# Optimization experiments

Measured on AMD Instinct MI355X. Metric: run time of the kernel, lower is better.

## Reference

```python
import jax, jax.numpy as jnp
import numpy as np

DIM = 384
HEADS = 12
WS = (2, 7, 7)
SS = (1, 3, 3)


def _rel_position_index(ws):
    coords = np.stack(np.meshgrid(np.arange(ws[0]), np.arange(ws[1]), np.arange(ws[2]), indexing='ij'))
    cf = coords.reshape(3, -1)                      # (3, N)
    rc = cf[:, :, None] - cf[:, None, :]            # (3, N, N)
    rc = rc.transpose(1, 2, 0).astype(np.int64)     # (N, N, 3)
    rc[..., 0] += ws[0] - 1
    rc[..., 1] += ws[1] - 1
    rc[..., 2] += ws[2] - 1
    rc[..., 0] *= (2 * ws[1] - 1) * (2 * ws[2] - 1)
    rc[..., 1] *= 2 * ws[2] - 1
    return rc.sum(-1)                               # (N, N)


def _compute_mask(D, H, W, ws, ss):
    img = np.zeros((1, D, H, W, 1), np.float32)
    cnt = 0
    for d in (slice(0, -ws[0]), slice(-ws[0], -ss[0]), slice(-ss[0], None)):
        for h in (slice(0, -ws[1]), slice(-ws[1], -ss[1]), slice(-ss[1], None)):
            for w in (slice(0, -ws[2]), slice(-ws[2], -ss[2]), slice(-ss[2], None)):
                img[:, d, h, w, :] = cnt
                cnt += 1
    x = img.reshape(1, D // ws[0], ws[0], H // ws[1], ws[1], W // ws[2], ws[2], 1)
    mw = x.transpose(0, 1, 3, 5, 2, 4, 6, 7).reshape(-1, ws[0] * ws[1] * ws[2])  # (nW, N)
    am = mw[:, None, :] - mw[:, :, None]
    return jnp.asarray(np.where(am != 0, -100.0, 0.0).astype(np.float32))  # (nW, N, N)


def _window_partition(x, ws):
    B, D, H, W, C = x.shape
    x = x.reshape(B, D // ws[0], ws[0], H // ws[1], ws[1], W // ws[2], ws[2], C)
    return x.transpose(0, 1, 3, 5, 2, 4, 6, 7).reshape(-1, ws[0] * ws[1] * ws[2], C)


def _window_reverse(win, ws, B, D, H, W):
    x = win.reshape(B, D // ws[0], H // ws[1], W // ws[2], ws[0], ws[1], ws[2], -1)
    return x.transpose(0, 1, 4, 2, 5, 3, 6, 7).reshape(B, D, H, W, -1)


def _ln(x, g, b, eps=1e-5):
    mu = x.mean(-1, keepdims=True)
    var = ((x - mu) ** 2).mean(-1, keepdims=True)
    return (x - mu) * jax.lax.rsqrt(var + eps) * g + b


def setup_inputs() -> dict:
    key = jax.random.key(0)
    ks = jax.random.split(key, 8)
    C = DIM
    Ch = int(4.0 * C)
    s = lambda k, shape: jax.random.normal(k, shape, dtype=jnp.float32) * 0.02
    nbias = (2 * WS[0] - 1) * (2 * WS[1] - 1) * (2 * WS[2] - 1)
    return dict(
        x=jax.random.normal(ks[0], (4, 8, 56, 56, C), dtype=jnp.float32),
        norm1_g=jnp.ones((C,), jnp.float32), norm1_b=jnp.zeros((C,), jnp.float32),
        qkv_w=s(ks[1], (3 * C, C)), qkv_b=jnp.zeros((3 * C,), jnp.float32),
        rpb_table=s(ks[2], (nbias, HEADS)),
        proj_w=s(ks[3], (C, C)), proj_b=jnp.zeros((C,), jnp.float32),
        norm2_g=jnp.ones((C,), jnp.float32), norm2_b=jnp.zeros((C,), jnp.float32),
        fc1_w=s(ks[4], (Ch, C)), fc1_b=jnp.zeros((Ch,), jnp.float32),
        fc2_w=s(ks[5], (C, Ch)), fc2_b=jnp.zeros((C,), jnp.float32),
    )


def reference(x, norm1_g, norm1_b, qkv_w, qkv_b, rpb_table, proj_w, proj_b,
              norm2_g, norm2_b, fc1_w, fc1_b, fc2_w, fc2_b):
    B, D, H, W, C = x.shape
    ws, ss = WS, SS
    hd = C // HEADS
    N = ws[0] * ws[1] * ws[2]

    shortcut = x
    h = _ln(x, norm1_g, norm1_b)
    # cyclic shift (no padding needed: D,H,W are window multiples)
    h = jnp.roll(h, shift=(-ss[0], -ss[1], -ss[2]), axis=(1, 2, 3))
    xw = _window_partition(h, ws)                       # (B_, N, C)
    B_ = xw.shape[0]

    qkv = (xw @ qkv_w.T + qkv_b).reshape(B_, N, 3, HEADS, hd).transpose(2, 0, 3, 1, 4)
    q, k, v = qkv[0], qkv[1], qkv[2]                    # (B_, heads, N, hd)
    attn = jnp.einsum('bhnd,bhmd->bhnm', q * (hd ** -0.5), k)

    rpi = _rel_position_index(ws)                       # (N, N) static
    bias = rpb_table[rpi.reshape(-1)].reshape(N, N, HEADS).transpose(2, 0, 1)
    attn = attn + bias[None]

    mask = _compute_mask(D, H, W, ws, ss)               # (nW, N, N)
    nW = mask.shape[0]
    attn = attn.reshape(B_ // nW, nW, HEADS, N, N) + mask[None, :, None]
    attn = jax.nn.softmax(attn.reshape(-1, HEADS, N, N), axis=-1)

    out = jnp.einsum('bhnm,bhmd->bhnd', attn, v).transpose(0, 2, 1, 3).reshape(B_, N, C)
    out = out @ proj_w.T + proj_b

    h = _window_reverse(out, ws, B, D, H, W)
    h = jnp.roll(h, shift=(ss[0], ss[1], ss[2]), axis=(1, 2, 3))
    x = shortcut + h

    y = _ln(x, norm2_g, norm2_b)
    y = jax.nn.gelu(y @ fc1_w.T + fc1_b, approximate=False) @ fc2_w.T + fc2_b
    return x + y
```

## Files before the change

kernel.cpp:

```cpp
#include <hip/hip_runtime.h>
#include <hip/hip_bf16.h>
#include <cmath>

typedef __hip_bfloat16 bf16;
typedef __attribute__((ext_vector_type(8))) short s16x8;
typedef __attribute__((ext_vector_type(4))) float f32x4v;

__device__ __forceinline__ float bf2f(bf16 v){ return __bfloat162float(v); }
__device__ __forceinline__ bf16  f2bf(float v){ return __float2bfloat16(v); }

__device__ __forceinline__ void gload16(const void* g, void* l){
  __builtin_amdgcn_global_load_lds((const __attribute__((address_space(1))) void*)g,
                                   (__attribute__((address_space(3))) void*)l,
                                   16, 0, 0);
}

__device__ __forceinline__ int xcd_swizzle(int bid, int nb){
  int q = nb >> 3, r = nb & 7;
  int xcd = bid & 7, idx = bid >> 3;
  return (xcd < r) ? (xcd*(q+1) + idx) : (r + xcd*q + idx);
}

__device__ __forceinline__ float gelu_f(float v){
  float y = 0.797884561f*(v + 0.044715f*v*v*v);
  float e = __expf(-2.f*y);
  return v * __builtin_amdgcn_rcpf(1.f + e);
}

__global__ void k_f2bf(const float* __restrict__ in, bf16* __restrict__ out, int n){
  int i = blockIdx.x*256 + threadIdx.x;
  if (i < n) out[i] = f2bf(in[i]);
}

__global__ void k_comb(const float* __restrict__ rpb, float* __restrict__ comb){
  int idx = blockIdx.x*256 + threadIdx.x;
  int col = idx & 127, row = (idx>>7)&127, clshead = idx>>14;
  int cls = clshead/12, head = clshead - cls*12;
  float v;
  if (row >= 98) v = 0.f;
  else if (col >= 98) v = -10000.f;
  else {
    int qd = row/49, qr = row%49, qh = qr/7, qw = qr%7;
    int kd = col/49, kr = col%49, kh = kr/7, kw = kr%7;
    int pbq = qd*169 + qh*13 + qw;
    int pbk = kd*169 + kh*13 + kw;
    int lq, lk;
    {
      int ld = (cls&4) ? (qd==0?1:2) : 0;
      int lh = (cls&2) ? (qh<4?1:2) : 0;
      int lw = (cls&1) ? (qw<4?1:2) : 0;
      lq = ld*9+lh*3+lw;
    }
    {
      int ld = (cls&4) ? (kd==0?1:2) : 0;
      int lh = (cls&2) ? (kh<4?1:2) : 0;
      int lw = (cls&1) ? (kw<4?1:2) : 0;
      lk = ld*9+lh*3+lw;
    }
    float bias = rpb[(pbq-pbk+253)*12 + head];
    v = bias + ((lq!=lk) ? -100.f : 0.f);
  }
  comb[idx] = v;
}

__global__ __launch_bounds__(256)
void k_ln1(const float* __restrict__ x, const float* __restrict__ g,
           const float* __restrict__ b, bf16* __restrict__ xw, long tbase)
{
  int tl = blockIdx.x*4 + (threadIdx.x>>6);
  long t = tbase + tl;
  int lane = threadIdx.x & 63;
  int win = (int)(t / 98), n = (int)(t % 98);
  int batch = win>>8;
  int wq = win & 7, hq = (win>>3)&7, dq = (win>>6)&3;
  int dr = n/49, rem = n%49, hr = rem/7, wr = rem%7;
  int d = dq*2+dr, h = hq*7+hr, w = wq*7+wr;
  int sd = (d+1)&7;
  int sh = h+3; if (sh>=56) sh-=56;
  int sw = w+3; if (sw>=56) sw-=56;
  const float* row = x + ((size_t)(((batch*8+sd)*56+sh)*56+sw))*384;
  float v[6]; float s=0.f, ss=0.f;
  int c0 = lane*6;
  #pragma unroll
  for (int i=0;i<6;++i){ float f = row[c0+i]; v[i]=f; s+=f; ss+=f*f; }
  #pragma unroll
  for (int o=32;o>0;o>>=1){ s += __shfl_xor(s,o); ss += __shfl_xor(ss,o); }
  float mu = s*(1.f/384.f);
  float var = ss*(1.f/384.f) - mu*mu;
  float rstd = rsqrtf(var + 1e-5f);
  bf16* orow = xw + (size_t)tl*384;
  #pragma unroll
  for (int i=0;i<6;++i){ int c=c0+i; orow[c] = f2bf((v[i]-mu)*rstd*g[c] + b[c]); }
}

__global__ __launch_bounds__(256)
void k_scatter_ln2(const bf16* __restrict__ projout, const float* __restrict__ x,
                   const float* __restrict__ g, const float* __restrict__ b,
                   float* __restrict__ x2, bf16* __restrict__ ln2,
                   long tbase, long lnbase)
{
  int tl = blockIdx.x*4 + (threadIdx.x>>6);
  long t = tbase + tl;
  int lane = threadIdx.x & 63;
  int win = (int)(t/98), n = (int)(t%98);
  int batch = win>>8;
  int wq = win&7, hq=(win>>3)&7, dq=(win>>6)&3;
  int dr=n/49, rem=n%49, hr=rem/7, wr=rem%7;
  int d=dq*2+dr, h=hq*7+hr, w=wq*7+wr;
  int sd=(d+1)&7;
  int sh=h+3; if(sh>=56)sh-=56;
  int sw=w+3; if(sw>=56)sw-=56;
  size_t nat = (size_t)(sd*56+sh)*56 + sw;
  size_t nrow = (size_t)batch*25088 + nat;
  const float* xrow = x + nrow*384;
  const bf16* prow = projout + (size_t)tl*384;
  float* x2row = x2 + nrow*384;
  bf16* lrow = ln2 + (nrow - (size_t)lnbase)*384;
  int c0 = lane*6;
  float v[6]; float s=0.f, ss=0.f;
  #pragma unroll
  for (int i=0;i<6;++i){
    float f = xrow[c0+i] + bf2f(prow[c0+i]);
    v[i]=f; s+=f; ss+=f*f;
    x2row[c0+i] = f;
  }
  #pragma unroll
  for (int o=32;o>0;o>>=1){ s+=__shfl_xor(s,o); ss+=__shfl_xor(ss,o); }
  float mu=s*(1.f/384.f), var=ss*(1.f/384.f)-mu*mu, rstd=rsqrtf(var+1e-5f);
  #pragma unroll
  for (int i=0;i<6;++i){ int c=c0+i; lrow[c]=f2bf((v[i]-mu)*rstd*g[c]+b[c]); }
}

template<int EPI, int KT>
__global__ __launch_bounds__(256, 2)
void k_gemm(const bf16* __restrict__ A, const bf16* __restrict__ B,
            const float* __restrict__ bias, const float* __restrict__ resid,
            void* __restrict__ outp, int N, int nx)
{
  constexpr int K = KT*32;
  __shared__ __align__(16) bf16 As[2][256*32];
  __shared__ __align__(16) bf16 Bs[2][128*32];
  const int tid = threadIdx.x;
  const int wave = tid>>6, lane = tid&63;
  const int wg = xcd_swizzle(blockIdx.x, gridDim.x);
  const int tn = wg % nx, tm = wg / nx;
  const int wm = wave>>1, wn = wave&1;
  const int fr = lane & 15, l4 = lane>>4;

  f32x4v acc[8][4];
  #pragma unroll
  for (int i=0;i<8;++i)
    #pragma unroll
    for (int j=0;j<4;++j)
      #pragma unroll
      for (int e=0;e<4;++e) acc[i][j][e] = 0.f;

  const int srow0 = lane>>2;
  const int scol_sw = (((lane&3) ^ ((lane>>3)&3)))*8;
  const bf16* gA = A + ((size_t)tm*256 + wave*16 + srow0)*K + scol_sw;
  const bf16* gB = B + ((size_t)tn*128 + wave*16 + srow0)*K + scol_sw;

  auto stage = [&](int buf, int koff){
    #pragma unroll
    for (int j=0;j<4;++j)
      gload16(gA + (size_t)(64*j)*K + koff, &As[buf][j*2048 + wave*512]);
    #pragma unroll
    for (int j=0;j<2;++j)
      gload16(gB + (size_t)(64*j)*K + koff, &Bs[buf][j*2048 + wave*512]);
  };

  stage(0, 0);

  const int fko_sw = ((l4 ^ ((fr>>1)&3)))*8;

  #pragma unroll 2
  for (int kt=0; kt<KT; ++kt){
    asm volatile("s_waitcnt vmcnt(0) lgkmcnt(0)" ::: "memory");
    __builtin_amdgcn_s_barrier();
    if (kt+1 < KT) stage((kt+1)&1, (kt+1)*32);
    const bf16* Ab = As[kt&1];
    const bf16* Bb = Bs[kt&1];
    s16x8 af[8], bfr[4];
    #pragma unroll
    for (int i=0;i<4;++i)
      bfr[i] = *(const s16x8*)&Bb[(wn*64 + i*16 + fr)*32 + fko_sw];
    #pragma unroll
    for (int i=0;i<8;++i)
      af[i] = *(const s16x8*)&Ab[(wm*128 + i*16 + fr)*32 + fko_sw];
    #pragma unroll
    for (int mi=0;mi<8;++mi)
      #pragma unroll
      for (int ni=0;ni<4;++ni)
        acc[mi][ni] = __builtin_amdgcn_mfma_f32_16x16x32_bf16(af[mi], bfr[ni], acc[mi][ni], 0,0,0);
    __builtin_amdgcn_s_barrier();
  }

  #pragma unroll
  for (int mi=0;mi<8;++mi){
    #pragma unroll
    for (int ni=0;ni<4;++ni){
      int col = tn*128 + wn*64 + ni*16 + fr;
      float bv = bias[col];
      int rowb = tm*256 + wm*128 + mi*16 + l4*4;
      #pragma unroll
      for (int r=0;r<4;++r){
        size_t idx = (size_t)(rowb+r)*N + col;
        float v = acc[mi][ni][r] + bv;
        if (EPI==0){
          ((bf16*)outp)[idx] = f2bf(v);
        } else if (EPI==1){
          ((bf16*)outp)[idx] = f2bf(gelu_f(v));
        } else if (EPI==3){
          if (col < 384) v *= 0.17677669529663687f;
          ((bf16*)outp)[idx] = f2bf(v);
        } else {
          ((float*)outp)[idx] = v + resid[idx];
        }
      }
    }
  }
}

__global__ __launch_bounds__(256)
void k_attn(const bf16* __restrict__ qkv, const float* __restrict__ comb,
            bf16* __restrict__ outp)
{
  const int wg   = xcd_swizzle(blockIdx.x, gridDim.x);
  const int head = wg % 12;
  const int win  = wg / 12;
  const int tid  = threadIdx.x;
  const int wave = tid>>6;
  const int lane = tid&63;
  const int l15 = lane & 15, l4 = lane>>4;
  __shared__ __align__(16) bf16 Vt[32*136];
  __shared__ __align__(16) bf16 P_buf[4][16*40];

  const int wq = win&7, hq=(win>>3)&7, dq=(win>>6)&3;
  const int cls = ((dq==3)?4:0) | ((hq==7)?2:0) | ((wq==7)?1:0);
  const float* combbase = comb + (size_t)(cls*12+head)*128*128;
  const bf16* qkvw_ = qkv + (size_t)win*98*1152;

  for (int i = tid; i < 512; i += 256){
    int m = i>>2, d0 = (i&3)*8;
    int mc = m>97 ? 97 : m;
    s16x8 v = *(const s16x8*)(qkvw_ + (size_t)mc*1152 + 768 + head*32 + d0);
    #pragma unroll
    for (int e=0;e<8;++e){ short sv = v[e]; Vt[(d0+e)*136 + m] = *(bf16*)&sv; }
  }
  s16x8 kb[8];
  #pragma unroll
  for (int j=0;j<8;++j){
    int tok = j*16 + l15; if (tok>97) tok = 97;
    kb[j] = *(const s16x8*)(qkvw_ + (size_t)tok*1152 + 384 + head*32 + l4*8);
  }
  __syncthreads();

  const int c0 = wave*32;
  bf16* Pw = P_buf[wave];
  #pragma unroll
  for (int mi=0;mi<2;++mi){
    int q = c0 + mi*16 + l15; if (q>97) q=97;
    s16x8 aq = *(const s16x8*)(qkvw_ + (size_t)q*1152 + head*32 + l4*8);
    f32x4v s[8];
    const float* cb = combbase + (size_t)(c0+mi*16+l4*4)*128 + l15;
    #pragma unroll
    for (int j=0;j<8;++j){
      f32x4v ci = { cb[j*16], cb[j*16+128], cb[j*16+256], cb[j*16+384] };
      s[j] = __builtin_amdgcn_mfma_f32_16x16x32_bf16(aq, kb[j], ci, 0,0,0);
    }
    float rinv[4];
    #pragma unroll
    for (int r=0;r<4;++r){
      float mx = s[0][r];
      #pragma unroll
      for (int j=1;j<8;++j) mx = fmaxf(mx, s[j][r]);
      mx = fmaxf(mx, __shfl_xor(mx,1));
      mx = fmaxf(mx, __shfl_xor(mx,2));
      mx = fmaxf(mx, __shfl_xor(mx,4));
      mx = fmaxf(mx, __shfl_xor(mx,8));
      float sum = 0.f;
      #pragma unroll
      for (int j=0;j<8;++j){ float e = __expf(s[j][r]-mx); s[j][r]=e; sum+=e; }
      sum += __shfl_xor(sum,1);
      sum += __shfl_xor(sum,2);
      sum += __shfl_xor(sum,4);
      sum += __shfl_xor(sum,8);
      rinv[r] = 1.f/sum;
    }
    f32x4v oacc[2] = {{0.f,0.f,0.f,0.f},{0.f,0.f,0.f,0.f}};
    #pragma unroll
    for (int ks=0; ks<4; ++ks){
      #pragma unroll
      for (int jj=0;jj<2;++jj)
        #pragma unroll
        for (int r=0;r<4;++r)
          Pw[(l4*4+r)*40 + jj*16 + l15] = f2bf(s[ks*2+jj][r]);
      s16x8 pa = *(const s16x8*)&Pw[l15*40 + l4*8];
      #pragma unroll
      for (int ni=0;ni<2;++ni){
        s16x8 vb = *(const s16x8*)&Vt[(ni*16+l15)*136 + ks*32 + l4*8];
        oacc[ni] = __builtin_amdgcn_mfma_f32_16x16x32_bf16(pa, vb, oacc[ni], 0,0,0);
      }
    }
    #pragma unroll
    for (int r=0;r<4;++r){
      int qo = c0 + mi*16 + l4*4 + r;
      if (qo < 98){
        bf16* orow = outp + ((size_t)win*98 + qo)*384 + head*32;
        #pragma unroll
        for (int ni=0;ni<2;++ni)
          orow[ni*16+l15] = f2bf(oacc[ni][r]*rinv[r]);
      }
    }
  }
}

extern "C" void kernel_launch(void* const* d_in, const int* in_sizes, int n_in,
                              void* d_out, int out_size, void* d_ws, size_t ws_size,
                              hipStream_t stream)
{
  const float* x     = (const float*)d_in[0];
  const float* n1g   = (const float*)d_in[1];
  const float* n1b   = (const float*)d_in[2];
  const float* qkvw  = (const float*)d_in[3];
  const float* qkvbv = (const float*)d_in[4];
  const float* rpb   = (const float*)d_in[5];
  const float* projw = (const float*)d_in[6];
  const float* projb = (const float*)d_in[7];
  const float* n2g   = (const float*)d_in[8];
  const float* n2b   = (const float*)d_in[9];
  const float* fc1w  = (const float*)d_in[10];
  const float* fc1b  = (const float*)d_in[11];
  const float* fc2w  = (const float*)d_in[12];
  const float* fc2b  = (const float*)d_in[13];
  float* out = (float*)d_out;

  char* ws = (char*)d_ws;
  size_t off = 0;
  auto alloc = [&](size_t bytes)->char*{
    char* p = ws + off; off += (bytes + 255) & ~(size_t)255; return p;
  };
  bf16*  wqkv  = (bf16*)alloc((size_t)1152*384*2);
  bf16*  wproj = (bf16*)alloc((size_t)384*384*2);
  bf16*  wfc1  = (bf16*)alloc((size_t)1536*384*2);
  bf16*  wfc2  = (bf16*)alloc((size_t)384*1536*2);
  float* comb  = (float*)alloc((size_t)96*128*128*4);

  k_f2bf<<<(1152*384+255)/256,256,0,stream>>>(qkvw, wqkv, 1152*384);
  k_f2bf<<<(384*384+255)/256,256,0,stream>>>(projw, wproj, 384*384);
  k_f2bf<<<(1536*384+255)/256,256,0,stream>>>(fc1w, wfc1, 1536*384);
  k_f2bf<<<(384*1536+255)/256,256,0,stream>>>(fc2w, wfc2, 384*1536);
  k_comb<<<6144,256,0,stream>>>(rpb, comb);

  const size_t fused_need = off + ((size_t)100352*384*2 + 255 & ~(size_t)255)
                                + ((size_t)100352*1536*2 + 255 & ~(size_t)255)
                                + ((size_t)100352*384*2 + 255 & ~(size_t)255);
  if (ws_size >= fused_need){
    bf16* xw   = (bf16*)alloc((size_t)100352*384*2);
    bf16* bufA = (bf16*)alloc((size_t)100352*1536*2);
    bf16* ln2  = (bf16*)alloc((size_t)100352*384*2);
    bf16* attno = bufA + (size_t)100352*1152;
    bf16* projo = xw;

    k_ln1<<<25088,256,0,stream>>>(x, n1g, n1b, xw, 0L);
    k_gemm<3,12><<<392*9,256,0,stream>>>(xw, wqkv, qkvbv, nullptr, bufA, 1152, 9);
    k_attn<<<12*1024,256,0,stream>>>(bufA, comb, attno);
    k_gemm<0,12><<<392*3,256,0,stream>>>(attno, wproj, projb, nullptr, projo, 384, 3);
    k_scatter_ln2<<<25088,256,0,stream>>>(projo, x, n2g, n2b, out, ln2, 0L, 0L);
    k_gemm<1,12><<<392*12,256,0,stream>>>(ln2, wfc1, fc1b, nullptr, bufA, 1536, 12);
    k_gemm<2,48><<<392*3,256,0,stream>>>(bufA, wfc2, fc2b, out, (void*)out, 384, 3);
  } else {
    bf16* xw   = (bf16*)alloc((size_t)25088*384*2);
    bf16* bufA = (bf16*)alloc((size_t)25088*1536*2);
    bf16* ln2  = (bf16*)alloc((size_t)25088*384*2);
    bf16* attno = bufA + (size_t)25088*1152;
    bf16* projo = xw;
    for (int b=0; b<4; ++b){
      long tbase = (long)b*25088;
      k_ln1<<<6272,256,0,stream>>>(x, n1g, n1b, xw, tbase);
      k_gemm<3,12><<<98*9,256,0,stream>>>(xw, wqkv, qkvbv, nullptr, bufA, 1152, 9);
      k_attn<<<12*256,256,0,stream>>>(bufA, comb, attno);
      k_gemm<0,12><<<98*3,256,0,stream>>>(attno, wproj, projb, nullptr, projo, 384, 3);
      k_scatter_ln2<<<6272,256,0,stream>>>(projo, x, n2g, n2b, out, ln2, tbase, tbase);
      k_gemm<1,12><<<98*12,256,0,stream>>>(ln2, wfc1, fc1b, nullptr, bufA, 1536, 12);
      float* resid = out + (size_t)b*25088*384;
      k_gemm<2,48><<<98*3,256,0,stream>>>(bufA, wfc2, fc2b, resid, (void*)resid, 384, 3);
    }
  }
}
```

Measured before the change: 954.3 us.

## Fuse projection GEMM with residual add, window reverse and LayerNorm2

Replaces the projection GEMM plus separate scatter/LN2 kernel with one 512-thread kernel where each block computes 128 full rows of 384 output columns. It adds bias and the shortcut, writes the residual to its unshifted position, reduces row statistics through shared memory and writes the normalized bf16 LN2 input. This removes the bf16 projection intermediate round trip and one launch. The four weight-conversion launches are also merged into one. The cost is a large per-block tile with one block per CU, which may reduce occupancy and overlap.

```diff
diff --git a/kernel.cpp b/kernel.cpp
--- a/kernel.cpp
+++ b/kernel.cpp
@@ -27,9 +27,17 @@
   return v * __builtin_amdgcn_rcpf(1.f + e);
 }
 
-__global__ void k_f2bf(const float* __restrict__ in, bf16* __restrict__ out, int n){
+__global__ void k_f2bf4(const float* __restrict__ s0, const float* __restrict__ s1,
+                        const float* __restrict__ s2, const float* __restrict__ s3,
+                        bf16* __restrict__ out){
   int i = blockIdx.x*256 + threadIdx.x;
-  if (i < n) out[i] = f2bf(in[i]);
+  if (i >= 1769472) return;
+  float v;
+  if      (i <  442368) v = s0[i];
+  else if (i <  589824) v = s1[i -  442368];
+  else if (i < 1179648) v = s2[i -  589824];
+  else                  v = s3[i - 1179648];
+  out[i] = f2bf(v);
 }
 
 __global__ void k_comb(const float* __restrict__ rpb, float* __restrict__ comb){
@@ -93,44 +101,6 @@
   for (int i=0;i<6;++i){ int c=c0+i; orow[c] = f2bf((v[i]-mu)*rstd*g[c] + b[c]); }
 }
 
-__global__ __launch_bounds__(256)
-void k_scatter_ln2(const bf16* __restrict__ projout, const float* __restrict__ x,
-                   const float* __restrict__ g, const float* __restrict__ b,
-                   float* __restrict__ x2, bf16* __restrict__ ln2,
-                   long tbase, long lnbase)
-{
-  int tl = blockIdx.x*4 + (threadIdx.x>>6);
-  long t = tbase + tl;
-  int lane = threadIdx.x & 63;
-  int win = (int)(t/98), n = (int)(t%98);
-  int batch = win>>8;
-  int wq = win&7, hq=(win>>3)&7, dq=(win>>6)&3;
-  int dr=n/49, rem=n%49, hr=rem/7, wr=rem%7;
-  int d=dq*2+dr, h=hq*7+hr, w=wq*7+wr;
-  int sd=(d+1)&7;
-  int sh=h+3; if(sh>=56)sh-=56;
-  int sw=w+3; if(sw>=56)sw-=56;
-  size_t nat = (size_t)(sd*56+sh)*56 + sw;
-  size_t nrow = (size_t)batch*25088 + nat;
-  const float* xrow = x + nrow*384;
-  const bf16* prow = projout + (size_t)tl*384;
-  float* x2row = x2 + nrow*384;
-  bf16* lrow = ln2 + (nrow - (size_t)lnbase)*384;
-  int c0 = lane*6;
-  float v[6]; float s=0.f, ss=0.f;
-  #pragma unroll
-  for (int i=0;i<6;++i){
-    float f = xrow[c0+i] + bf2f(prow[c0+i]);
-    v[i]=f; s+=f; ss+=f*f;
-    x2row[c0+i] = f;
-  }
-  #pragma unroll
-  for (int o=32;o>0;o>>=1){ s+=__shfl_xor(s,o); ss+=__shfl_xor(ss,o); }
-  float mu=s*(1.f/384.f), var=ss*(1.f/384.f)-mu*mu, rstd=rsqrtf(var+1e-5f);
-  #pragma unroll
-  for (int i=0;i<6;++i){ int c=c0+i; lrow[c]=f2bf((v[i]-mu)*rstd*g[c]+b[c]); }
-}
-
 template<int EPI, int KT>
 __global__ __launch_bounds__(256, 2)
 void k_gemm(const bf16* __restrict__ A, const bf16* __restrict__ B,
@@ -221,6 +191,136 @@
   }
 }
 
+template<int KT>
+__global__ __launch_bounds__(512, 1)
+void k_projln2(const bf16* __restrict__ A, const bf16* __restrict__ B,
+               const float* __restrict__ bias, const float* __restrict__ x,
+               const float* __restrict__ g, const float* __restrict__ b2,
+               float* __restrict__ outx, bf16* __restrict__ ln2,
+               long tbase, long lnbase)
+{
+  constexpr int K = KT*32;
+  __shared__ __align__(16) bf16 As[2][128*32];
+  __shared__ __align__(16) bf16 Bs[2][384*32];
+  __shared__ float redS[128][4];
+  __shared__ float redQ[128][4];
+  const int tid = threadIdx.x;
+  const int wave = tid>>6, lane = tid&63;
+  const int tm = xcd_swizzle(blockIdx.x, gridDim.x);
+  const int wm = wave>>2, wn = wave&3;
+  const int fr = lane & 15, l4 = lane>>4;
+
+  f32x4v acc[4][6];
+  #pragma unroll
+  for (int i=0;i<4;++i)
+    #pragma unroll
+    for (int j=0;j<6;++j)
+      #pragma unroll
+      for (int e=0;e<4;++e) acc[i][j][e] = 0.f;
+
+  const int srow0 = lane>>2;
+  const int scol_sw = (((lane&3) ^ ((lane>>3)&3)))*8;
+  const bf16* gA = A + ((size_t)tm*128 + wave*16 + srow0)*K + scol_sw;
+  const bf16* gB = B + ((size_t)(wave*16) + srow0)*K + scol_sw;
+
+  auto stage = [&](int buf, int koff){
+    gload16(gA + koff, &As[buf][wave*512]);
+    #pragma unroll
+    for (int j=0;j<3;++j)
+      gload16(gB + (size_t)(128*j)*K + koff, &Bs[buf][(j*128 + wave*16)*32]);
+  };
+
+  stage(0, 0);
+  const int fko_sw = ((l4 ^ ((fr>>1)&3)))*8;
+
+  #pragma unroll 2
+  for (int kt=0; kt<KT; ++kt){
+    asm volatile("s_waitcnt vmcnt(0) lgkmcnt(0)" ::: "memory");
+    __builtin_amdgcn_s_barrier();
+    if (kt+1 < KT) stage((kt+1)&1, (kt+1)*32);
+    const bf16* Ab = As[kt&1];
+    const bf16* Bb = Bs[kt&1];
+    s16x8 af[4], bfr[6];
+    #pragma unroll
+    for (int i=0;i<6;++i)
+      bfr[i] = *(const s16x8*)&Bb[(wn*96 + i*16 + fr)*32 + fko_sw];
+    #pragma unroll
+    for (int i=0;i<4;++i)
+      af[i] = *(const s16x8*)&Ab[(wm*64 + i*16 + fr)*32 + fko_sw];
+    #pragma unroll
+    for (int mi=0;mi<4;++mi)
+      #pragma unroll
+      for (int ni=0;ni<6;++ni)
+        acc[mi][ni] = __builtin_amdgcn_mfma_f32_16x16x32_bf16(af[mi], bfr[ni], acc[mi][ni], 0,0,0);
+    __builtin_amdgcn_s_barrier();
+  }
+
+  float bv[6];
+  #pragma unroll
+  for (int ni=0;ni<6;++ni) bv[ni] = bias[wn*96 + ni*16 + fr];
+
+  long nr[4][4];
+  #pragma unroll
+  for (int mi=0;mi<4;++mi){
+    #pragma unroll
+    for (int r=0;r<4;++r){
+      int lrow = wm*64 + mi*16 + l4*4 + r;
+      int ti = (int)(tbase + (long)tm*128 + lrow);
+      int win = ti/98, n = ti - win*98;
+      int batch = win>>8;
+      int wq = win&7, hq = (win>>3)&7, dq = (win>>6)&3;
+      int dr = n/49, rem = n - dr*49, hr = rem/7, wr = rem - hr*7;
+      int d = dq*2+dr, h = hq*7+hr, w = wq*7+wr;
+      int sd = (d+1)&7;
+      int sh = h+3; if (sh>=56) sh-=56;
+      int sw = w+3; if (sw>=56) sw-=56;
+      long nrow = (long)batch*25088 + (long)(sd*56+sh)*56 + sw;
+      nr[mi][r] = nrow;
+      const float* xrow = x + (size_t)nrow*384;
+      float* orow = outx + (size_t)nrow*384;
+      float s = 0.f, q = 0.f;
+      #pragma unroll
+      for (int ni=0;ni<6;++ni){
+        int col = wn*96 + ni*16 + fr;
+        float hvl = acc[mi][ni][r] + bv[ni] + xrow[col];
+        orow[col] = hvl;
+        acc[mi][ni][r] = hvl;
+        s += hvl; q += hvl*hvl;
+      }
+      s += __shfl_xor(s,1); q += __shfl_xor(q,1);
+      s += __shfl_xor(s,2); q += __shfl_xor(q,2);
+      s += __shfl_xor(s,4); q += __shfl_xor(q,4);
+      s += __shfl_xor(s,8); q += __shfl_xor(q,8);
+      if (fr == 0){ redS[lrow][wn] = s; redQ[lrow][wn] = q; }
+    }
+  }
+  __syncthreads();
+  float gv[6], b2v[6];
+  #pragma unroll
+  for (int ni=0;ni<6;++ni){
+    int col = wn*96 + ni*16 + fr;
+    gv[ni] = g[col]; b2v[ni] = b2[col];
+  }
+  #pragma unroll
+  for (int mi=0;mi<4;++mi){
+    #pragma unroll
+    for (int r=0;r<4;++r){
+      int lrow = wm*64 + mi*16 + l4*4 + r;
+      float S = redS[lrow][0] + redS[lrow][1] + redS[lrow][2] + redS[lrow][3];
+      float Q = redQ[lrow][0] + redQ[lrow][1] + redQ[lrow][2] + redQ[lrow][3];
+      float mu = S*(1.f/384.f);
+      float var = Q*(1.f/384.f) - mu*mu;
+      float rstd = rsqrtf(var + 1e-5f);
+      bf16* lrowp = ln2 + (size_t)(nr[mi][r] - lnbase)*384;
+      #pragma unroll
+      for (int ni=0;ni<6;++ni){
+        int col = wn*96 + ni*16 + fr;
+        lrowp[col] = f2bf((acc[mi][ni][r] - mu)*rstd*gv[ni] + b2v[ni]);
+      }
+    }
+  }
+}
+
 __global__ __launch_bounds__(256)
 void k_attn(const bf16* __restrict__ qkv, const float* __restrict__ comb,
             bf16* __restrict__ outp)
@@ -243,7 +343,7 @@
   for (int i = tid; i < 512; i += 256){
     int m = i>>2, d0 = (i&3)*8;
     int mc = m>97 ? 97 : m;
-    s16x8 v = *(const s16x8*)(qkvw_ + (size_t)mc*1152 + 768 + head*32 + d0);
+    s16x8 v = *(const s16x8*)(qkvw_ + (size_t)mc*1152 + 384 + 384 + head*32 + d0);
     #pragma unroll
     for (int e=0;e<8;++e){ short sv = v[e]; Vt[(d0+e)*136 + m] = *(bf16*)&sv; }
   }
@@ -340,33 +440,30 @@
   auto alloc = [&](size_t bytes)->char*{
     char* p = ws + off; off += (bytes + 255) & ~(size_t)255; return p;
   };
-  bf16*  wqkv  = (bf16*)alloc((size_t)1152*384*2);
-  bf16*  wproj = (bf16*)alloc((size_t)384*384*2);
-  bf16*  wfc1  = (bf16*)alloc((size_t)1536*384*2);
-  bf16*  wfc2  = (bf16*)alloc((size_t)384*1536*2);
+  bf16*  wall  = (bf16*)alloc((size_t)1769472*2);
+  bf16*  wqkv  = wall;
+  bf16*  wproj = wall + 442368;
+  bf16*  wfc1  = wall + 589824;
+  bf16*  wfc2  = wall + 1179648;
   float* comb  = (float*)alloc((size_t)96*128*128*4);
 
-  k_f2bf<<<(1152*384+255)/256,256,0,stream>>>(qkvw, wqkv, 1152*384);
-  k_f2bf<<<(384*384+255)/256,256,0,stream>>>(projw, wproj, 384*384);
-  k_f2bf<<<(1536*384+255)/256,256,0,stream>>>(fc1w, wfc1, 1536*384);
-  k_f2bf<<<(384*1536+255)/256,256,0,stream>>>(fc2w, wfc2, 384*1536);
+  k_f2bf4<<<(1769472+255)/256,256,0,stream>>>(qkvw, projw, fc1w, fc2w, wall);
   k_comb<<<6144,256,0,stream>>>(rpb, comb);
 
-  const size_t fused_need = off + ((size_t)100352*384*2 + 255 & ~(size_t)255)
-                                + ((size_t)100352*1536*2 + 255 & ~(size_t)255)
-                                + ((size_t)100352*384*2 + 255 & ~(size_t)255);
+  const size_t fused_need = off
+      + (((size_t)100352*384*2  + 255) & ~(size_t)255)
+      + (((size_t)100352*1536*2 + 255) & ~(size_t)255)
+      + (((size_t)100352*384*2  + 255) & ~(size_t)255);
   if (ws_size >= fused_need){
     bf16* xw   = (bf16*)alloc((size_t)100352*384*2);
     bf16* bufA = (bf16*)alloc((size_t)100352*1536*2);
     bf16* ln2  = (bf16*)alloc((size_t)100352*384*2);
     bf16* attno = bufA + (size_t)100352*1152;
-    bf16* projo = xw;
 
     k_ln1<<<25088,256,0,stream>>>(x, n1g, n1b, xw, 0L);
     k_gemm<3,12><<<392*9,256,0,stream>>>(xw, wqkv, qkvbv, nullptr, bufA, 1152, 9);
     k_attn<<<12*1024,256,0,stream>>>(bufA, comb, attno);
-    k_gemm<0,12><<<392*3,256,0,stream>>>(attno, wproj, projb, nullptr, projo, 384, 3);
-    k_scatter_ln2<<<25088,256,0,stream>>>(projo, x, n2g, n2b, out, ln2, 0L, 0L);
+    k_projln2<12><<<784,512,0,stream>>>(attno, wproj, projb, x, n2g, n2b, out, ln2, 0L, 0L);
     k_gemm<1,12><<<392*12,256,0,stream>>>(ln2, wfc1, fc1b, nullptr, bufA, 1536, 12);
     k_gemm<2,48><<<392*3,256,0,stream>>>(bufA, wfc2, fc2b, out, (void*)out, 384, 3);
   } else {
@@ -374,14 +471,12 @@
     bf16* bufA = (bf16*)alloc((size_t)25088*1536*2);
     bf16* ln2  = (bf16*)alloc((size_t)25088*384*2);
     bf16* attno = bufA + (size_t)25088*1152;
-    bf16* projo = xw;
     for (int b=0; b<4; ++b){
       long tbase = (long)b*25088;
       k_ln1<<<6272,256,0,stream>>>(x, n1g, n1b, xw, tbase);
       k_gemm<3,12><<<98*9,256,0,stream>>>(xw, wqkv, qkvbv, nullptr, bufA, 1152, 9);
       k_attn<<<12*256,256,0,stream>>>(bufA, comb, attno);
-      k_gemm<0,12><<<98*3,256,0,stream>>>(attno, wproj, projb, nullptr, projo, 384, 3);
-      k_scatter_ln2<<<6272,256,0,stream>>>(projo, x, n2g, n2b, out, ln2, tbase, tbase);
+      k_projln2<12><<<196,512,0,stream>>>(attno, wproj, projb, x, n2g, n2b, out, ln2, tbase, tbase);
       k_gemm<1,12><<<98*12,256,0,stream>>>(ln2, wfc1, fc1b, nullptr, bufA, 1536, 12);
       float* resid = out + (size_t)b*25088*384;
       k_gemm<2,48><<<98*3,256,0,stream>>>(bufA, wfc2, fc2b, resid, (void*)resid, 384, 3);
```

New measurement: 968.3 us. No clear change (+1.5%).
